# Kernel tuning notes

Measured on AMD Instinct MI355X. Metric: run time of the kernel, lower is better.

Reference implementation:

```python
import jax, jax.numpy as jnp
import numpy as np

NUM_RBF = 300
RADIUS_RES = 0.1
GAMMA = 10.0
HIDDEN = 64
MB, ATOM = 32, 64


def setup_inputs() -> dict:
    key = jax.random.key(0)
    ks = jax.random.split(key, 12)
    def lin(kw, kb, fan_in, fan_out):
        lim = 1.0 / np.sqrt(fan_in)
        W = jax.random.uniform(kw, (fan_out, fan_in), jnp.float32, -lim, lim)
        b = jax.random.uniform(kb, (fan_out,), jnp.float32, -lim, lim)
        return W, b
    W1, b1 = lin(ks[0], ks[1], HIDDEN, HIDDEN)
    W2, b2 = lin(ks[2], ks[3], HIDDEN, HIDDEN)
    W3, b3 = lin(ks[4], ks[5], HIDDEN, HIDDEN)
    Wd1, bd1 = lin(ks[6], ks[7], NUM_RBF, HIDDEN)
    Wd2, bd2 = lin(ks[8], ks[9], HIDDEN, HIDDEN)
    x = jax.random.normal(ks[10], (MB, ATOM, HIDDEN), jnp.float32)
    dist = jax.random.uniform(ks[11], (MB, ATOM, ATOM), jnp.float32, 0.0, 10.0)
    return {"x": x, "dist": dist,
            "W1": W1, "b1": b1, "W2": W2, "b2": b2, "W3": W3, "b3": b3,
            "Wd1": Wd1, "bd1": bd1, "Wd2": Wd2, "bd2": bd2}


def reference(x, dist, W1, b1, W2, b2, W3, b3, Wd1, bd1, Wd2, bd2):
    sp = jax.nn.softplus
    # linear1 applied per-atom
    v = jnp.einsum('mic,oc->mio', x, W1) + b1                      # [mb, atom, h]
    # CFConv: gaussian RBF expansion of pairwise distances
    centers = jnp.arange(NUM_RBF, dtype=jnp.float32) * RADIUS_RES  # [rbf]
    rbf = jnp.exp(-GAMMA * (dist[..., None] - centers) ** 2)       # [mb, a, a, rbf]
    # 2-layer filter MLP on each pair
    f = sp(jnp.einsum('mijr,hr->mijh', rbf, Wd1) + bd1)            # [mb, a, a, h]
    f = sp(jnp.einsum('mijh,oh->mijo', f, Wd2) + bd2)              # [mb, a, a, h]
    # broadcast-multiply v over pairs and reduce over source atom i (dim=1)
    v = jnp.einsum('mic,mijc->mjc', v, f)                          # [mb, atom, h]
    v = sp(jnp.einsum('mic,oc->mio', v, W2) + b2)
    v = jnp.einsum('mic,oc->mio', v, W3) + b3
    return x + v
```

## Files before the change

kernel.cpp:

```cpp
#include <hip/hip_runtime.h>
#include <math.h>

#define MB_    32
#define ATOM_  64
#define HID_   64
#define NRBF_  300
#define GAMMA_ 10.0f
#define RES_   0.1f

#define TPTS      2001
#define TSTEP     0.005f
#define INV_TSTEP 200.0f

#define T_OFF   0
#define T_SZ    (TPTS * 64)
#define V1_OFF  (T_OFF + T_SZ)
#define V1_SZ   (MB_ * 64 * 64)
#define W2T_OFF (V1_OFF + V1_SZ)
#define W3T_OFF (W2T_OFF + 4096)

__device__ __forceinline__ float sp_f(float x) {
    return fmaxf(x, 0.f) + log1pf(__expf(-fabsf(x)));
}

__global__ __launch_bounds__(256)
void schnet_prep(const float* __restrict__ x,   const float* __restrict__ W1,
                 const float* __restrict__ b1,  const float* __restrict__ W2,
                 const float* __restrict__ W3,  const float* __restrict__ Wd1,
                 const float* __restrict__ bd1, const float* __restrict__ Wd2,
                 const float* __restrict__ bd2, float* __restrict__ ws)
{
    __shared__ float smem[8256];
    const int tid = threadIdx.x;
    const int b   = blockIdx.x;

    if (b < MB_) {
        float* sx = smem;
        float* sw = smem + 4096;
        const float* xm = x + b * 4096;
        for (int e = tid; e < 1024; e += 256)
            ((float4*)sx)[e] = ((const float4*)xm)[e];
        for (int e = tid; e < 4096; e += 256) {
            int o = e >> 6, c = e & 63;
            sw[c * 65 + o] = W1[e];
        }
        __syncthreads();
        const int o = tid & 63, p = tid >> 6;
        const float bo = b1[o];
        for (int ii = 0; ii < 16; ++ii) {
            const int i = p * 16 + ii;
            float acc = bo;
            #pragma unroll
            for (int c = 0; c < 64; ++c)
                acc = fmaf(sx[i * 64 + c], sw[c * 65 + o], acc);
            ws[V1_OFF + (b * 64 + i) * 64 + o] = acc;
        }
    } else if (b < MB_ + 501) {
        float* rbf = smem;
        float* u   = smem + 1280;
        float* wt  = smem + 1536;
        const int sub = tid >> 6, lane = tid & 63;
        const int s = (b - MB_) * 4 + sub;
        const bool live = (s < TPTS);
        const float d = live ? s * TSTEP : 0.f;

        if (live) {
            for (int r = lane; r < NRBF_; r += 64) {
                float t = fmaf(-RES_, (float)r, d);
                rbf[sub * 320 + r] = __expf(-GAMMA_ * t * t);
            }
            if (lane < 20) rbf[sub * 320 + 300 + lane] = 0.f;
        }
        float a = live ? bd1[lane] : 0.f;
        for (int r0 = 0; r0 < 320; r0 += 64) {
            __syncthreads();
            for (int e = tid; e < 4096; e += 256) {
                int h = e >> 6, rr = e & 63;
                int r = r0 + rr;
                wt[rr * 65 + h] = (r < NRBF_) ? Wd1[h * NRBF_ + r] : 0.f;
            }
            __syncthreads();
            if (live) {
                #pragma unroll
                for (int rr = 0; rr < 64; ++rr)
                    a = fmaf(wt[rr * 65 + lane], rbf[sub * 320 + r0 + rr], a);
            }
        }
        if (live) u[sub * 64 + lane] = sp_f(a);
        __syncthreads();
        for (int e = tid; e < 4096; e += 256) {
            int o = e >> 6, c = e & 63;
            wt[c * 65 + o] = Wd2[e];
        }
        __syncthreads();
        if (live) {
            float a2 = bd2[lane];
            #pragma unroll
            for (int h1 = 0; h1 < 64; ++h1)
                a2 = fmaf(wt[h1 * 65 + lane], u[sub * 64 + h1], a2);
            ws[T_OFF + s * 64 + lane] = sp_f(a2);
        }
    } else {
        for (int e = tid; e < 4096; e += 256) {
            int o = e >> 6, c = e & 63;
            ws[W2T_OFF + c * 64 + o] = W2[e];
            ws[W3T_OFF + c * 64 + o] = W3[e];
        }
    }
}

__global__ __launch_bounds__(256)
void schnet_main(const float* __restrict__ x, const float* __restrict__ dist,
                 const float* __restrict__ b2, const float* __restrict__ b3,
                 const float* __restrict__ ws, float* __restrict__ out)
{
    __shared__ float sD[64];
    __shared__ float sRed[4 * 64];
    const int m   = blockIdx.x >> 6;
    const int j   = blockIdx.x & 63;
    const int tid = threadIdx.x;
    const int c   = tid & 63;
    const int p   = tid >> 6;

    if (tid < 64) sD[tid] = dist[(m * ATOM_ + tid) * ATOM_ + j];
    __syncthreads();

    const float* Tb  = ws + T_OFF;
    const float* v1m = ws + V1_OFF + (m * 64 + p * 16) * 64;
    float acc = 0.f;
    #pragma unroll
    for (int ii = 0; ii < 16; ++ii) {
        float d  = sD[p * 16 + ii];
        float f  = d * INV_TSTEP;
        int   s  = min((int)f, TPTS - 2);
        float fr = f - (float)s;
        const float* Tr = Tb + s * 64;
        float t0 = Tr[c], t1 = Tr[64 + c];
        float f2v = fmaf(fr, t1 - t0, t0);
        acc = fmaf(f2v, v1m[ii * 64 + c], acc);
    }
    sRed[p * 64 + c] = acc;
    __syncthreads();
    if (tid < 64)
        sD[tid] = sRed[tid] + sRed[64 + tid] + sRed[128 + tid] + sRed[192 + tid];
    __syncthreads();

    {
        const float* W2t = ws + W2T_OFF;
        float s_ = 0.f;
        #pragma unroll
        for (int cc = 0; cc < 16; ++cc)
            s_ = fmaf(sD[16 * p + cc], W2t[(16 * p + cc) * 64 + c], s_);
        sRed[p * 64 + c] = s_;
    }
    __syncthreads();
    if (tid < 64)
        sD[tid] = sp_f(sRed[tid] + sRed[64 + tid] + sRed[128 + tid] + sRed[192 + tid] + b2[tid]);
    __syncthreads();
    {
        const float* W3t = ws + W3T_OFF;
        float s_ = 0.f;
        #pragma unroll
        for (int cc = 0; cc < 16; ++cc)
            s_ = fmaf(sD[16 * p + cc], W3t[(16 * p + cc) * 64 + c], s_);
        sRed[p * 64 + c] = s_;
    }
    __syncthreads();
    if (tid < 64) {
        float v_ = sRed[tid] + sRed[64 + tid] + sRed[128 + tid] + sRed[192 + tid] + b3[tid];
        out[(m * ATOM_ + j) * HID_ + tid] = v_ + x[(m * ATOM_ + j) * HID_ + tid];
    }
}

extern "C" void kernel_launch(void* const* d_in, const int* in_sizes, int n_in,
                              void* d_out, int out_size, void* d_ws, size_t ws_size,
                              hipStream_t stream) {
    const float* x   = (const float*)d_in[0];
    const float* dist= (const float*)d_in[1];
    const float* W1  = (const float*)d_in[2];
    const float* b1  = (const float*)d_in[3];
    const float* W2  = (const float*)d_in[4];
    const float* b2  = (const float*)d_in[5];
    const float* W3  = (const float*)d_in[6];
    const float* b3  = (const float*)d_in[7];
    const float* Wd1 = (const float*)d_in[8];
    const float* bd1 = (const float*)d_in[9];
    const float* Wd2 = (const float*)d_in[10];
    const float* bd2 = (const float*)d_in[11];
    float* out = (float*)d_out;
    float* ws  = (float*)d_ws;
    (void)in_sizes; (void)n_in; (void)out_size; (void)ws_size;

    schnet_prep<<<dim3(MB_ + 501 + 1), dim3(256), 0, stream>>>(
        x, W1, b1, W2, W3, Wd1, bd1, Wd2, bd2, ws);
    schnet_main<<<dim3(MB_ * ATOM_), dim3(256), 0, stream>>>(
        x, dist, b2, b3, ws, out);
}
```

Before: 104.9 us.

## Interleave filter table pairs for float2 lookups, shuffle distances, split FMA chains

The precomputed filter table is stored with each entry's value and its next-step neighbor interleaved, so the main kernel fetches both interpolation endpoints with one float2 load instead of two scalar loads. Distances are now read into registers and broadcast with wavefront shuffles, which removes a shared-memory stage and a barrier. The prep kernel's dot products use two accumulators to shorten dependency chains. In exchange the table doubles in size and writes are duplicated, and the float2 path depends on the table offset being 8-byte aligned.

```diff
diff --git a/kernel.cpp b/kernel.cpp
--- a/kernel.cpp
+++ b/kernel.cpp
@@ -13,7 +13,7 @@
 #define INV_TSTEP 200.0f
 
 #define T_OFF   0
-#define T_SZ    (TPTS * 64)
+#define T_SZ    (TPTS * 128)
 #define V1_OFF  (T_OFF + T_SZ)
 #define V1_SZ   (MB_ * 64 * 64)
 #define W2T_OFF (V1_OFF + V1_SZ)
@@ -49,11 +49,13 @@
         const float bo = b1[o];
         for (int ii = 0; ii < 16; ++ii) {
             const int i = p * 16 + ii;
-            float acc = bo;
+            float a0 = bo, a1 = 0.f;
             #pragma unroll
-            for (int c = 0; c < 64; ++c)
-                acc = fmaf(sx[i * 64 + c], sw[c * 65 + o], acc);
-            ws[V1_OFF + (b * 64 + i) * 64 + o] = acc;
+            for (int c = 0; c < 64; c += 2) {
+                a0 = fmaf(sx[i * 64 + c],     sw[c * 65 + o],       a0);
+                a1 = fmaf(sx[i * 64 + c + 1], sw[(c + 1) * 65 + o], a1);
+            }
+            ws[V1_OFF + (b * 64 + i) * 64 + o] = a0 + a1;
         }
     } else if (b < MB_ + 501) {
         float* rbf = smem;
@@ -71,7 +73,7 @@
             }
             if (lane < 20) rbf[sub * 320 + 300 + lane] = 0.f;
         }
-        float a = live ? bd1[lane] : 0.f;
+        float a0 = live ? bd1[lane] : 0.f, a1 = 0.f;
         for (int r0 = 0; r0 < 320; r0 += 64) {
             __syncthreads();
             for (int e = tid; e < 4096; e += 256) {
@@ -82,11 +84,13 @@
             __syncthreads();
             if (live) {
                 #pragma unroll
-                for (int rr = 0; rr < 64; ++rr)
-                    a = fmaf(wt[rr * 65 + lane], rbf[sub * 320 + r0 + rr], a);
-            }
-        }
-        if (live) u[sub * 64 + lane] = sp_f(a);
+                for (int rr = 0; rr < 64; rr += 2) {
+                    a0 = fmaf(wt[rr * 65 + lane],       rbf[sub * 320 + r0 + rr],     a0);
+                    a1 = fmaf(wt[(rr + 1) * 65 + lane], rbf[sub * 320 + r0 + rr + 1], a1);
+                }
+            }
+        }
+        if (live) u[sub * 64 + lane] = sp_f(a0 + a1);
         __syncthreads();
         for (int e = tid; e < 4096; e += 256) {
             int o = e >> 6, c = e & 63;
@@ -94,11 +98,15 @@
         }
         __syncthreads();
         if (live) {
-            float a2 = bd2[lane];
+            float c0 = bd2[lane], c1 = 0.f;
             #pragma unroll
-            for (int h1 = 0; h1 < 64; ++h1)
-                a2 = fmaf(wt[h1 * 65 + lane], u[sub * 64 + h1], a2);
-            ws[T_OFF + s * 64 + lane] = sp_f(a2);
+            for (int h1 = 0; h1 < 64; h1 += 2) {
+                c0 = fmaf(wt[h1 * 65 + lane],       u[sub * 64 + h1],     c0);
+                c1 = fmaf(wt[(h1 + 1) * 65 + lane], u[sub * 64 + h1 + 1], c1);
+            }
+            float val = sp_f(c0 + c1);
+            ws[T_OFF + s * 128 + 2 * lane] = val;
+            if (s > 0) ws[T_OFF + (s - 1) * 128 + 2 * lane + 1] = val;
         }
     } else {
         for (int e = tid; e < 4096; e += 256) {
@@ -114,35 +122,33 @@
                  const float* __restrict__ b2, const float* __restrict__ b3,
                  const float* __restrict__ ws, float* __restrict__ out)
 {
-    __shared__ float sD[64];
     __shared__ float sRed[4 * 64];
+    __shared__ float sAgg[64];
     const int m   = blockIdx.x >> 6;
     const int j   = blockIdx.x & 63;
     const int tid = threadIdx.x;
     const int c   = tid & 63;
     const int p   = tid >> 6;
 
-    if (tid < 64) sD[tid] = dist[(m * ATOM_ + tid) * ATOM_ + j];
-    __syncthreads();
+    float dv = dist[(m * ATOM_ + p * 16 + (c & 15)) * ATOM_ + j];
 
     const float* Tb  = ws + T_OFF;
     const float* v1m = ws + V1_OFF + (m * 64 + p * 16) * 64;
     float acc = 0.f;
     #pragma unroll
     for (int ii = 0; ii < 16; ++ii) {
-        float d  = sD[p * 16 + ii];
+        float d  = __shfl(dv, ii, 64);
         float f  = d * INV_TSTEP;
         int   s  = min((int)f, TPTS - 2);
         float fr = f - (float)s;
-        const float* Tr = Tb + s * 64;
-        float t0 = Tr[c], t1 = Tr[64 + c];
-        float f2v = fmaf(fr, t1 - t0, t0);
+        float2 tv = *(const float2*)(Tb + s * 128 + 2 * c);
+        float f2v = fmaf(fr, tv.y - tv.x, tv.x);
         acc = fmaf(f2v, v1m[ii * 64 + c], acc);
     }
     sRed[p * 64 + c] = acc;
     __syncthreads();
     if (tid < 64)
-        sD[tid] = sRed[tid] + sRed[64 + tid] + sRed[128 + tid] + sRed[192 + tid];
+        sAgg[tid] = sRed[tid] + sRed[64 + tid] + sRed[128 + tid] + sRed[192 + tid];
     __syncthreads();
 
     {
@@ -150,19 +156,19 @@
         float s_ = 0.f;
         #pragma unroll
         for (int cc = 0; cc < 16; ++cc)
-            s_ = fmaf(sD[16 * p + cc], W2t[(16 * p + cc) * 64 + c], s_);
+            s_ = fmaf(sAgg[16 * p + cc], W2t[(16 * p + cc) * 64 + c], s_);
         sRed[p * 64 + c] = s_;
     }
     __syncthreads();
     if (tid < 64)
-        sD[tid] = sp_f(sRed[tid] + sRed[64 + tid] + sRed[128 + tid] + sRed[192 + tid] + b2[tid]);
+        sAgg[tid] = sp_f(sRed[tid] + sRed[64 + tid] + sRed[128 + tid] + sRed[192 + tid] + b2[tid]);
     __syncthreads();
     {
         const float* W3t = ws + W3T_OFF;
         float s_ = 0.f;
         #pragma unroll
         for (int cc = 0; cc < 16; ++cc)
-            s_ = fmaf(sD[16 * p + cc], W3t[(16 * p + cc) * 64 + c], s_);
+            s_ = fmaf(sAgg[16 * p + cc], W3t[(16 * p + cc) * 64 + c], s_);
         sRed[p * 64 + c] = s_;
     }
     __syncthreads();
```

After: 121.2 us. 1.16x slower.

## Truncate RBF sum to a window near each distance and register-tile linear1

Applied to the files above, without the earlier changes.

The filter-table prep now sums only the 28 RBF centers near each table distance, since the Gaussian with gamma 10 is negligible farther out. This replaces the full 300-term dot product and the shared-memory staging of Wd1 with direct global reads. The second filter layer reads Wd2 rows as float4 straight from global memory, and the linear1 GEMM now uses a 4x4 register tile per thread over padded shared tiles. Truncating the window adds a small approximation error and produces uncoalesced row-strided global loads.

```diff
diff --git a/kernel.cpp b/kernel.cpp
--- a/kernel.cpp
+++ b/kernel.cpp
@@ -11,6 +11,8 @@
 #define TPTS      2001
 #define TSTEP     0.005f
 #define INV_TSTEP 200.0f
+
+#define RWIN 28
 
 #define T_OFF   0
 #define T_SZ    (TPTS * 64)
@@ -30,76 +32,83 @@
                  const float* __restrict__ bd1, const float* __restrict__ Wd2,
                  const float* __restrict__ bd2, float* __restrict__ ws)
 {
-    __shared__ float smem[8256];
+    __shared__ float smem[8320];
     const int tid = threadIdx.x;
     const int b   = blockIdx.x;
 
     if (b < MB_) {
         float* sx = smem;
-        float* sw = smem + 4096;
+        float* sw = smem + 4160;
         const float* xm = x + b * 4096;
-        for (int e = tid; e < 1024; e += 256)
-            ((float4*)sx)[e] = ((const float4*)xm)[e];
         for (int e = tid; e < 4096; e += 256) {
-            int o = e >> 6, c = e & 63;
-            sw[c * 65 + o] = W1[e];
+            int i = e >> 6, c = e & 63;
+            sx[i * 65 + c] = xm[e];
+            sw[i * 65 + c] = W1[e];
         }
         __syncthreads();
-        const int o = tid & 63, p = tid >> 6;
-        const float bo = b1[o];
-        for (int ii = 0; ii < 16; ++ii) {
-            const int i = p * 16 + ii;
-            float acc = bo;
-            #pragma unroll
-            for (int c = 0; c < 64; ++c)
-                acc = fmaf(sx[i * 64 + c], sw[c * 65 + o], acc);
-            ws[V1_OFF + (b * 64 + i) * 64 + o] = acc;
+        const int tx = tid & 15;
+        const int ty = tid >> 4;
+        float acc[4][4];
+        #pragma unroll
+        for (int aa = 0; aa < 4; ++aa)
+            #pragma unroll
+            for (int bb = 0; bb < 4; ++bb)
+                acc[aa][bb] = b1[4 * tx + bb];
+        #pragma unroll 8
+        for (int k = 0; k < 64; ++k) {
+            float xa[4], wb[4];
+            #pragma unroll
+            for (int aa = 0; aa < 4; ++aa) xa[aa] = sx[(4 * ty + aa) * 65 + k];
+            #pragma unroll
+            for (int bb = 0; bb < 4; ++bb) wb[bb] = sw[(4 * tx + bb) * 65 + k];
+            #pragma unroll
+            for (int aa = 0; aa < 4; ++aa)
+                #pragma unroll
+                for (int bb = 0; bb < 4; ++bb)
+                    acc[aa][bb] = fmaf(xa[aa], wb[bb], acc[aa][bb]);
+        }
+        #pragma unroll
+        for (int aa = 0; aa < 4; ++aa) {
+            float4 v = make_float4(acc[aa][0], acc[aa][1], acc[aa][2], acc[aa][3]);
+            *(float4*)(ws + V1_OFF + (b * 64 + 4 * ty + aa) * 64 + 4 * tx) = v;
         }
     } else if (b < MB_ + 501) {
-        float* rbf = smem;
-        float* u   = smem + 1280;
-        float* wt  = smem + 1536;
-        const int sub = tid >> 6, lane = tid & 63;
-        const int s = (b - MB_) * 4 + sub;
-        const bool live = (s < TPTS);
-        const float d = live ? s * TSTEP : 0.f;
-
-        if (live) {
-            for (int r = lane; r < NRBF_; r += 64) {
-                float t = fmaf(-RES_, (float)r, d);
-                rbf[sub * 320 + r] = __expf(-GAMMA_ * t * t);
-            }
-            if (lane < 20) rbf[sub * 320 + 300 + lane] = 0.f;
-        }
-        float a = live ? bd1[lane] : 0.f;
-        for (int r0 = 0; r0 < 320; r0 += 64) {
-            __syncthreads();
-            for (int e = tid; e < 4096; e += 256) {
-                int h = e >> 6, rr = e & 63;
-                int r = r0 + rr;
-                wt[rr * 65 + h] = (r < NRBF_) ? Wd1[h * NRBF_ + r] : 0.f;
-            }
-            __syncthreads();
-            if (live) {
-                #pragma unroll
-                for (int rr = 0; rr < 64; ++rr)
-                    a = fmaf(wt[rr * 65 + lane], rbf[sub * 320 + r0 + rr], a);
-            }
-        }
-        if (live) u[sub * 64 + lane] = sp_f(a);
+        float* su = smem;
+        const int sub = tid >> 6, c = tid & 63;
+        const int s  = (b - MB_) * 4 + sub;
+        const int se = min(s, TPTS - 1);
+        const float d = se * TSTEP;
+
+        int r0 = (int)ceilf((d - 1.35f) * 10.0f);
+        r0 = max(r0, 0);
+
+        float a0 = bd1[c], a1 = 0.f;
+        const float* wrow1 = Wd1 + c * NRBF_ + r0;
+        #pragma unroll
+        for (int k = 0; k < RWIN; k += 2) {
+            float t0 = fmaf(-RES_, (float)(r0 + k),     d);
+            float t1 = fmaf(-RES_, (float)(r0 + k + 1), d);
+            float w0 = __expf(-GAMMA_ * t0 * t0);
+            float w1 = __expf(-GAMMA_ * t1 * t1);
+            a0 = fmaf(w0, wrow1[k],     a0);
+            a1 = fmaf(w1, wrow1[k + 1], a1);
+        }
+        su[sub * 64 + c] = sp_f(a0 + a1);
         __syncthreads();
-        for (int e = tid; e < 4096; e += 256) {
-            int o = e >> 6, c = e & 63;
-            wt[c * 65 + o] = Wd2[e];
-        }
-        __syncthreads();
-        if (live) {
-            float a2 = bd2[lane];
-            #pragma unroll
-            for (int h1 = 0; h1 < 64; ++h1)
-                a2 = fmaf(wt[h1 * 65 + lane], u[sub * 64 + h1], a2);
-            ws[T_OFF + s * 64 + lane] = sp_f(a2);
-        }
+
+        const float4* wrow2 = (const float4*)(Wd2 + c * 64);
+        const float*  uu    = su + sub * 64;
+        float s0 = bd2[c], s1 = 0.f, s2 = 0.f, s3 = 0.f;
+        #pragma unroll
+        for (int h4 = 0; h4 < 16; ++h4) {
+            float4 wv = wrow2[h4];
+            s0 = fmaf(wv.x, uu[4 * h4 + 0], s0);
+            s1 = fmaf(wv.y, uu[4 * h4 + 1], s1);
+            s2 = fmaf(wv.z, uu[4 * h4 + 2], s2);
+            s3 = fmaf(wv.w, uu[4 * h4 + 3], s3);
+        }
+        if (s < TPTS)
+            ws[T_OFF + s * 64 + c] = sp_f((s0 + s1) + (s2 + s3));
     } else {
         for (int e = tid; e < 4096; e += 256) {
             int o = e >> 6, c = e & 63;
```

Result: faster. 93.94 us (median of 2 runs) (-10.5%).
